# Kernel tuning notes

Measured on AMD Instinct MI355X. Metric: run time of the kernel, lower is better.

The kernel has to match this reference:

```python
import jax, jax.numpy as jnp
import numpy as np


def group_norm(x, g, b, groups, eps=1e-5):
    # x: (B, C, H, W), PyTorch GroupNorm semantics
    B, C, H, W = x.shape
    xr = x.reshape(B, groups, -1)
    m = xr.mean(-1, keepdims=True)
    v = xr.var(-1, keepdims=True)
    xn = ((xr - m) * jax.lax.rsqrt(v + eps)).reshape(B, C, H, W)
    return xn * g[:, None, None] + b[:, None, None]


def mamba(xs, in_w, conv_w, conv_b, xproj_w, dt_w, dt_b, A_log, D, out_w):
    # Standard Mamba block: in_proj -> causal depthwise conv -> SiLU ->
    # x_proj -> softplus(dt_proj) -> selective scan -> gate -> out_proj.
    Bsz, L, d = xs.shape
    di = in_w.shape[0] // 2
    r = dt_w.shape[1]
    n = A_log.shape[1]
    K = conv_w.shape[1]
    xz = xs @ in_w.T                           # (B, L, 2*di)
    xpart, z = xz[..., :di], xz[..., di:]
    xp = jnp.pad(xpart, ((0, 0), (K - 1, 0), (0, 0)))  # causal pad
    xc = conv_b + sum(xp[:, k:k + L, :] * conv_w[:, k] for k in range(K))
    xc = jax.nn.silu(xc)
    proj = xc @ xproj_w.T                      # (B, L, r + 2n)
    dt = proj[..., :r]
    Bm = proj[..., r:r + n]
    Cm = proj[..., r + n:]
    delta = jax.nn.softplus(dt @ dt_w.T + dt_b)   # (B, L, di)
    A = -jnp.exp(A_log)                            # (di, n)
    dA = jnp.exp(jnp.einsum('bld,dn->bldn', delta, A))
    dBu = jnp.einsum('bld,bln,bld->bldn', delta, Bm, xc)

    def step(h, inp):
        dA_t, dBu_t, C_t = inp
        h = dA_t * h + dBu_t                  # (B, di, n)
        return h, jnp.einsum('bdn,bn->bd', h, C_t)

    h0 = jnp.zeros((Bsz, di, n), xs.dtype)
    _, ys = jax.lax.scan(step, h0, (jnp.moveaxis(dA, 1, 0), jnp.moveaxis(dBu, 1, 0), jnp.moveaxis(Cm, 1, 0)))
    y = jnp.moveaxis(ys, 0, 1) + D * xc
    y = y * jax.nn.silu(z)
    return y @ out_w.T


def setup_inputs() -> dict:
    def nrm(i, shape, s=0.05):
        return jax.random.normal(jax.random.fold_in(jax.random.key(0), i), shape, dtype=jnp.float32) * s

    f32 = jnp.float32
    C = 128
    di, r, n = 256, 8, 16          # spa mamba: d_model=128, expand=2
    di2, r2 = 64, 2                # spe mamba: d_model=32
    A1 = jnp.log(jnp.broadcast_to(jnp.arange(1, n + 1, dtype=f32), (di, n)))
    A2 = jnp.log(jnp.broadcast_to(jnp.arange(1, n + 1, dtype=f32), (di2, n)))
    return {
        'x': nrm(0, (2, C, 64, 64), 1.0),
        'pe_w': nrm(1, (C, C)), 'pe_b': jnp.zeros((C,), f32),
        'pe_gn_g': jnp.ones((C,), f32), 'pe_gn_b': jnp.zeros((C,), f32),
        'spa_in_w': nrm(2, (2 * di, C)),
        'spa_conv_w': nrm(3, (di, 4)), 'spa_conv_b': jnp.zeros((di,), f32),
        'spa_xproj_w': nrm(4, (r + 2 * n, di)),
        'spa_dt_w': nrm(5, (di, r)), 'spa_dt_b': jnp.full((di,), -2.0, f32),
        'spa_Alog': A1, 'spa_D': jnp.ones((di,), f32),
        'spa_out_w': nrm(6, (C, di)),
        'spa_gn_g': jnp.ones((C,), f32), 'spa_gn_b': jnp.zeros((C,), f32),
        'spe_in_w': nrm(7, (2 * di2, 32)),
        'spe_conv_w': nrm(8, (di2, 4)), 'spe_conv_b': jnp.zeros((di2,), f32),
        'spe_xproj_w': nrm(9, (r2 + 2 * n, di2)),
        'spe_dt_w': nrm(10, (di2, r2)), 'spe_dt_b': jnp.full((di2,), -2.0, f32),
        'spe_Alog': A2, 'spe_D': jnp.ones((di2,), f32),
        'spe_out_w': nrm(11, (32, di2)),
        'spe_gn_g': jnp.ones((C,), f32), 'spe_gn_b': jnp.zeros((C,), f32),
        'fuse_w': jnp.full((2,), 0.5, f32),
        'cls_w': nrm(12, (10, C)), 'cls_b': jnp.zeros((10,), f32),
        'ref_dw_w': nrm(13, (C, 1, 3, 3)),
        'ref_gn_g': jnp.ones((C,), f32), 'ref_gn_b': jnp.zeros((C,), f32),
        'ref_pw_w': nrm(14, (1, C)), 'ref_pw_b': jnp.zeros((1,), f32),
        'alpha': jnp.asarray(1e-4, f32),
    }


def reference(x, pe_w, pe_b, pe_gn_g, pe_gn_b, spa_in_w, spa_conv_w, spa_conv_b, spa_xproj_w, spa_dt_w, spa_dt_b, spa_Alog, spa_D, spa_out_w, spa_gn_g, spa_gn_b, spe_in_w, spe_conv_w, spe_conv_b, spe_xproj_w, spe_dt_w, spe_dt_b, spe_Alog, spe_D, spe_out_w, spe_gn_g, spe_gn_b, fuse_w, cls_w, cls_b, ref_dw_w, ref_gn_g, ref_gn_b, ref_pw_w, ref_pw_b, alpha):
    B, _, H, W = x.shape
    # patch embedding: 1x1 conv + GroupNorm + SiLU
    h1 = jnp.einsum('bchw,oc->bohw', x, pe_w) + pe_b[:, None, None]
    h1 = jax.nn.silu(group_norm(h1, pe_gn_g, pe_gn_b, 4))
    # SpaMamba: scan over flattened spatial tokens (B, H*W, C)
    seq = h1.transpose(0, 2, 3, 1).reshape(B, H * W, -1)
    y = mamba(seq, spa_in_w, spa_conv_w, spa_conv_b, spa_xproj_w, spa_dt_w, spa_dt_b, spa_Alog, spa_D, spa_out_w)
    y = y.reshape(B, H, W, -1).transpose(0, 3, 1, 2)
    spa = jax.nn.silu(group_norm(y, spa_gn_g, spa_gn_b, 4)) + h1
    # SpeMamba: token_num=4, group_channel_num=32, channel_num=128 (no pad)
    seq2 = h1.transpose(0, 2, 3, 1).reshape(B * H * W, 4, 32)
    y2 = mamba(seq2, spe_in_w, spe_conv_w, spe_conv_b, spe_xproj_w, spe_dt_w, spe_dt_b, spe_Alog, spe_D, spe_out_w)
    y2 = y2.reshape(B, H, W, -1).transpose(0, 3, 1, 2)
    spe = h1 + jax.nn.silu(group_norm(y2, spe_gn_g, spe_gn_b, 4))
    # attention-weighted fusion + residual (BothMamba, use_att=True)
    wts = jax.nn.softmax(fuse_w)
    feat = spa * wts[0] + spe * wts[1] + h1
    # classifier head (1x1 conv)
    logits = jnp.einsum('bchw,oc->bohw', feat, cls_w) + cls_b[:, None, None]
    # BoundaryAwareLogitRefiner
    edge = jax.lax.conv_general_dilated(feat, ref_dw_w, (1, 1), ((1, 1), (1, 1)), feature_group_count=feat.shape[1], dimension_numbers=('NCHW', 'OIHW', 'NCHW'))
    edge = jax.nn.silu(group_norm(edge, ref_gn_g, ref_gn_b, 4))
    edge = jax.nn.sigmoid(jnp.einsum('bchw,oc->bohw', edge, ref_pw_w) + ref_pw_b[:, None, None])
    local = jax.lax.reduce_window(logits, 0.0, jax.lax.add, (1, 1, 3, 3), (1, 1, 1, 1), ((0, 0), (0, 0), (1, 1), (1, 1))) / 9.0  # count_include_pad=True
    return logits + alpha * (1.0 - edge) * (local - logits)
```

## Files before the change

kernel.cpp:

```cpp
#include <hip/hip_runtime.h>
#include <math.h>

#define DEV __device__ __forceinline__

DEV float sigm(float x){ return 1.f/(1.f+__expf(-x)); }
DEV float siluf(float x){ return x * sigm(x); }
DEV float softplusf(float x){ return x > 20.f ? x : log1pf(__expf(x)); }

static constexpr float NG = 131072.0f;
static constexpr float LOG2E = 1.4426950408889634f;

static constexpr size_t WS_H1    = 0;
static constexpr size_t WS_H1PRE = 1048576;
static constexpr size_t WS_XC    = 2097152;
static constexpr size_t WS_ZSIL  = 4194304;
static constexpr size_t WS_XZ    = 6291456;
static constexpr size_t WS_QOFF  = 6619136;
static constexpr size_t WS_LOG   = 8650752;
static constexpr size_t WS_Y     = 10485760;
static constexpr size_t WS_POFF  = 12582912;
static constexpr size_t WS_Y2    = 14155776;
static constexpr size_t WS_FEAT  = 15204352;
static constexpr size_t WS_STATS = 16252928;

__global__ void __launch_bounds__(256)
k_red(const float* __restrict__ part, float* __restrict__ outS, int half){
  __shared__ float red[4];
  int b = blockIdx.x >> 3, j = blockIdx.x & 7;
  float s = 0.f;
  for (int i = b*half + threadIdx.x; i < (b+1)*half; i += 256)
    s += part[(size_t)i*8 + j];
  s += __shfl_xor(s,1); s += __shfl_xor(s,2); s += __shfl_xor(s,4);
  s += __shfl_xor(s,8); s += __shfl_xor(s,16); s += __shfl_xor(s,32);
  if ((threadIdx.x & 63) == 0) red[threadIdx.x>>6] = s;
  __syncthreads();
  if (threadIdx.x == 0) outS[b*8+j] = red[0]+red[1]+red[2]+red[3];
}

__global__ void __launch_bounds__(256)
k_pe(const float* __restrict__ x, const float* __restrict__ pe_w,
     const float* __restrict__ pe_b, float* __restrict__ h1pre,
     float* __restrict__ part){
  __shared__ float As[16][36];
  __shared__ float Bs[16][64];
  __shared__ float red1[2][4], red2[2][4];
  int tid = threadIdx.x;
  int nx = blockIdx.x, my = blockIdx.y;
  int m0 = my*32, n0 = nx*64;
  int b = m0 >> 12, pl0 = m0 & 4095;
  int tx = tid & 15, ty = tid >> 4;
  float acc[2][4];
  #pragma unroll
  for (int i = 0; i < 2; i++)
    #pragma unroll
    for (int j = 0; j < 4; j++) acc[i][j] = 0.f;
  for (int k0 = 0; k0 < 128; k0 += 16){
    if (tid < 128){
      int k = tid >> 3, mm = (tid & 7)*4;
      float4 a = *(const float4*)(x + ((size_t)b*128 + k0+k)*4096 + pl0 + mm);
      *(float4*)&As[k][mm] = a;
    }
    {
      int n = tid >> 2, kq = (tid & 3)*4;
      float4 a = *(const float4*)(pe_w + (size_t)(n0+n)*128 + k0 + kq);
      Bs[kq+0][n] = a.x; Bs[kq+1][n] = a.y; Bs[kq+2][n] = a.z; Bs[kq+3][n] = a.w;
    }
    __syncthreads();
    #pragma unroll
    for (int k = 0; k < 16; k++){
      float2 av = *(const float2*)&As[k][ty*2];
      float4 bv = *(const float4*)&Bs[k][tx*4];
      acc[0][0] += av.x*bv.x; acc[0][1] += av.x*bv.y; acc[0][2] += av.x*bv.z; acc[0][3] += av.x*bv.w;
      acc[1][0] += av.y*bv.x; acc[1][1] += av.y*bv.y; acc[1][2] += av.y*bv.z; acc[1][3] += av.y*bv.w;
    }
    __syncthreads();
  }
  float4 bias = *(const float4*)(pe_b + n0 + tx*4);
  float s1 = 0.f, s2 = 0.f;
  #pragma unroll
  for (int i = 0; i < 2; i++){
    float4 st;
    st.x = acc[i][0]+bias.x; st.y = acc[i][1]+bias.y;
    st.z = acc[i][2]+bias.z; st.w = acc[i][3]+bias.w;
    s1 += st.x+st.y+st.z+st.w;
    s2 += st.x*st.x + st.y*st.y + st.z*st.z + st.w*st.w;
    *(float4*)(h1pre + (size_t)(m0 + ty*2 + i)*128 + n0 + tx*4) = st;
  }
  s1 += __shfl_xor(s1,1);  s2 += __shfl_xor(s2,1);
  s1 += __shfl_xor(s1,2);  s2 += __shfl_xor(s2,2);
  s1 += __shfl_xor(s1,4);  s2 += __shfl_xor(s2,4);
  s1 += __shfl_xor(s1,16); s2 += __shfl_xor(s2,16);
  s1 += __shfl_xor(s1,32); s2 += __shfl_xor(s2,32);
  int lane = tid & 63, w = tid >> 6;
  if ((lane & 55) == 0){
    int gl = (lane >> 3) & 1;
    red1[gl][w] = s1; red2[gl][w] = s2;
  }
  __syncthreads();
  if (tid < 8){
    int gg = tid >> 1, which = tid & 1;
    int gl = gg - nx*2;
    float v = 0.f;
    if (gl == 0 || gl == 1){
      v = which ? (red2[gl][0]+red2[gl][1]+red2[gl][2]+red2[gl][3])
                : (red1[gl][0]+red1[gl][1]+red1[gl][2]+red1[gl][3]);
    }
    int pblk = b*256 + (my & 127)*2 + nx;
    part[(size_t)pblk*8 + tid] = v;
  }
}

__global__ void __launch_bounds__(256)
k_xz(const float* __restrict__ h1pre, const float* __restrict__ in_w,
     const float* __restrict__ stats, const float* __restrict__ gng,
     const float* __restrict__ gnb, float* __restrict__ h1,
     float* __restrict__ xz, float* __restrict__ zsil){
  __shared__ float As[16][68];
  __shared__ float Bs[16][64];
  int tid = threadIdx.x;
  int m0 = blockIdx.y*64, n0 = blockIdx.x*64;
  int tx = tid & 15, ty = tid >> 4;
  float acc[4][4];
  #pragma unroll
  for (int i = 0; i < 4; i++)
    #pragma unroll
    for (int j = 0; j < 4; j++) acc[i][j] = 0.f;
  for (int k0 = 0; k0 < 128; k0 += 16){
    {
      int m = tid >> 2, kk = (tid & 3)*4;
      int pixm = m0 + m, c0 = k0 + kk;
      int bb = pixm >> 12, g = c0 >> 5;
      float4 a = *(const float4*)(h1pre + (size_t)pixm*128 + c0);
      float mu = stats[(bb*4+g)*2] * (1.f/NG);
      float var = stats[(bb*4+g)*2+1] * (1.f/NG) - mu*mu;
      float rs = rsqrtf(var + 1e-5f);
      float4 gg = *(const float4*)(gng + c0);
      float4 gb = *(const float4*)(gnb + c0);
      float4 v;
      v.x = siluf((a.x-mu)*rs*gg.x + gb.x);
      v.y = siluf((a.y-mu)*rs*gg.y + gb.y);
      v.z = siluf((a.z-mu)*rs*gg.z + gb.z);
      v.w = siluf((a.w-mu)*rs*gg.w + gb.w);
      As[kk+0][m] = v.x; As[kk+1][m] = v.y; As[kk+2][m] = v.z; As[kk+3][m] = v.w;
      if (blockIdx.x == 0) *(float4*)(h1 + (size_t)pixm*128 + c0) = v;
    }
    {
      int n = tid >> 2, kq = (tid & 3)*4;
      float4 a = *(const float4*)(in_w + (size_t)(n0+n)*128 + k0 + kq);
      Bs[kq+0][n] = a.x; Bs[kq+1][n] = a.y; Bs[kq+2][n] = a.z; Bs[kq+3][n] = a.w;
    }
    __syncthreads();
    #pragma unroll
    for (int k = 0; k < 16; k++){
      float4 av = *(const float4*)&As[k][ty*4];
      float4 bv = *(const float4*)&Bs[k][tx*4];
      acc[0][0] += av.x*bv.x; acc[0][1] += av.x*bv.y; acc[0][2] += av.x*bv.z; acc[0][3] += av.x*bv.w;
      acc[1][0] += av.y*bv.x; acc[1][1] += av.y*bv.y; acc[1][2] += av.y*bv.z; acc[1][3] += av.y*bv.w;
      acc[2][0] += av.z*bv.x; acc[2][1] += av.z*bv.y; acc[2][2] += av.z*bv.z; acc[2][3] += av.z*bv.w;
      acc[3][0] += av.w*bv.x; acc[3][1] += av.w*bv.y; acc[3][2] += av.w*bv.z; acc[3][3] += av.w*bv.w;
    }
    __syncthreads();
  }
  if (n0 < 256){
    #pragma unroll
    for (int i = 0; i < 4; i++){
      float4 st; st.x = acc[i][0]; st.y = acc[i][1]; st.z = acc[i][2]; st.w = acc[i][3];
      *(float4*)(xz + (size_t)(m0 + ty*4 + i)*512 + n0 + tx*4) = st;
    }
  } else {
    #pragma unroll
    for (int i = 0; i < 4; i++){
      float4 st;
      st.x = siluf(acc[i][0]); st.y = siluf(acc[i][1]);
      st.z = siluf(acc[i][2]); st.w = siluf(acc[i][3]);
      *(float4*)(zsil + (size_t)(m0 + ty*4 + i)*256 + (n0-256) + tx*4) = st;
    }
  }
}

__global__ void __launch_bounds__(256)
k_projc(const float* __restrict__ xz, const float* __restrict__ cw,
        const float* __restrict__ cb, const float* __restrict__ xpw,
        float* __restrict__ xc, float* __restrict__ proj){
  __shared__ float xct[16*260];
  int tid = threadIdx.x;
  int m0 = blockIdx.x * 16;
  {
    int slot = tid >> 6, lane = tid & 63;
    int d4 = lane*4;
    float4 cbv = *(const float4*)(cb + d4);
    float4 cw0 = *(const float4*)(cw + (size_t)(d4+0)*4);
    float4 cw1 = *(const float4*)(cw + (size_t)(d4+1)*4);
    float4 cw2 = *(const float4*)(cw + (size_t)(d4+2)*4);
    float4 cw3 = *(const float4*)(cw + (size_t)(d4+3)*4);
    const float* c0p = (const float*)&cw0;
    const float* c1p = (const float*)&cw1;
    const float* c2p = (const float*)&cw2;
    const float* c3p = (const float*)&cw3;
    for (int i = 0; i < 4; i++){
      int t = slot*4 + i;
      int tok = m0 + t;
      int l = tok & 4095;
      float4 acc = cbv;
      #pragma unroll
      for (int k = 0; k < 4; k++){
        int ls = l - 3 + k;
        if (ls >= 0){
          float4 xv = *(const float4*)(xz + (size_t)(tok-3+k)*512 + d4);
          acc.x += xv.x * c0p[k];
          acc.y += xv.y * c1p[k];
          acc.z += xv.z * c2p[k];
          acc.w += xv.w * c3p[k];
        }
      }
      float4 s;
      s.x = siluf(acc.x); s.y = siluf(acc.y); s.z = siluf(acc.z); s.w = siluf(acc.w);
      *(float4*)&xct[t*260 + d4] = s;
      *(float4*)(xc + (size_t)tok*256 + d4) = s;
    }
  }
  __syncthreads();
  {
    int t = tid & 15, jq = tid >> 4;
    int tok = m0 + t;
    float a0 = 0.f, a1 = 0.f, a2 = 0.f;
    for (int k0 = 0; k0 < 256; k0 += 4){
      float4 av = *(const float4*)&xct[t*260 + k0];
      float4 w0 = *(const float4*)(xpw + (size_t)jq*256 + k0);
      float4 w1 = *(const float4*)(xpw + (size_t)(jq+16)*256 + k0);
      a0 += av.x*w0.x + av.y*w0.y + av.z*w0.z + av.w*w0.w;
      a1 += av.x*w1.x + av.y*w1.y + av.z*w1.z + av.w*w1.w;
      if (jq < 8){
        float4 w2 = *(const float4*)(xpw + (size_t)(jq+32)*256 + k0);
        a2 += av.x*w2.x + av.y*w2.y + av.z*w2.z + av.w*w2.w;
      }
    }
    float* pr = proj + (size_t)tok*40;
    pr[jq] = a0;
    pr[jq+16] = a1;
    if (jq < 8) pr[jq+32] = a2;
  }
}

__global__ void __launch_bounds__(256)
k_delta(const float* __restrict__ proj, const float* __restrict__ dtw,
        const float* __restrict__ dtb, float* __restrict__ delta){
  int tid = threadIdx.x;
  int tok = blockIdx.x*4 + (tid >> 6);
  int lane = tid & 63;
  int d0 = lane*4;
  const float4* pr4 = (const float4*)(proj + (size_t)tok*40);
  float4 p0 = pr4[0], p1 = pr4[1];
  float4 outv;
  float* po = (float*)&outv;
  #pragma unroll
  for (int j = 0; j < 4; j++){
    int d = d0 + j;
    const float4* wr = (const float4*)(dtw + (size_t)d*8);
    float4 w0 = wr[0], w1 = wr[1];
    float v = dtb[d] + p0.x*w0.x + p0.y*w0.y + p0.z*w0.z + p0.w*w0.w
                     + p1.x*w1.x + p1.y*w1.y + p1.z*w1.z + p1.w*w1.w;
    po[j] = softplusf(v);
  }
  *(float4*)(delta + (size_t)tok*256 + d0) = outv;
}

__global__ void __launch_bounds__(256)
k_scan1(const float* __restrict__ delta, const float* __restrict__ proj,
        const float* __restrict__ xc, const float* __restrict__ Alog,
        float* __restrict__ P, float* __restrict__ Q){
  int blk = blockIdx.x;
  int dblk = blk & 3;
  int bc = blk >> 2;
  int b = bc >> 8, chunk = bc & 255;
  int tid = threadIdx.x;
  int dl = tid >> 2, ng = tid & 3;
  int d = dblk*64 + dl;
  float4 a4 = *(const float4*)(Alog + (size_t)d*16 + ng*4);
  float An[4] = {-__expf(a4.x)*LOG2E, -__expf(a4.y)*LOG2E,
                 -__expf(a4.z)*LOG2E, -__expf(a4.w)*LOG2E};
  float Pv[4] = {1.f,1.f,1.f,1.f}, Qv[4] = {0.f,0.f,0.f,0.f};
  size_t row0 = (size_t)(b*4096 + chunk*16);
  for (int l = 0; l < 16; l++){
    size_t r = row0 + l;
    float dv = delta[r*256 + d];
    float xv = xc[r*256 + d];
    float4 bm = *(const float4*)(proj + r*40 + 8 + ng*4);
    float dBx = dv*xv;
    float bmv[4] = {bm.x, bm.y, bm.z, bm.w};
    #pragma unroll
    for (int k = 0; k < 4; k++){
      float a = exp2f(dv*An[k]);
      Qv[k] = a*Qv[k] + bmv[k]*dBx;
      Pv[k] *= a;
    }
  }
  size_t o = (size_t)bc*4096 + dblk*1024 + tid*4;
  float4 pv; pv.x=Pv[0]; pv.y=Pv[1]; pv.z=Pv[2]; pv.w=Pv[3];
  float4 qv; qv.x=Qv[0]; qv.y=Qv[1]; qv.z=Qv[2]; qv.w=Qv[3];
  *(float4*)(P + o) = pv;
  *(float4*)(Q + o) = qv;
}

__global__ void __launch_bounds__(256)
k_scan2(const float* __restrict__ P, const float* __restrict__ Q,
        float* __restrict__ hs){
  __shared__ float Ps[256][17], Qs[256][17];
  int tid = threadIdx.x;
  int b = blockIdx.x >> 8;
  int dn0 = (blockIdx.x & 255) * 16;
  for (int i = tid; i < 1024; i += 256){
    int ch = i >> 2, g = (i & 3)*4;
    size_t gaddr = (size_t)(b*256+ch)*4096 + dn0 + g;
    float4 p = *(const float4*)(P + gaddr);
    float4 q = *(const float4*)(Q + gaddr);
    Ps[ch][g]=p.x; Ps[ch][g+1]=p.y; Ps[ch][g+2]=p.z; Ps[ch][g+3]=p.w;
    Qs[ch][g]=q.x; Qs[ch][g+1]=q.y; Qs[ch][g+2]=q.z; Qs[ch][g+3]=q.w;
  }
  __syncthreads();
  int lane = tid & 63, wv = tid >> 6;
  for (int rep = 0; rep < 4; rep++){
    int c = wv*4 + rep;
    float p0 = Ps[4*lane+0][c], q0 = Qs[4*lane+0][c];
    float p1 = Ps[4*lane+1][c], q1 = Qs[4*lane+1][c];
    float p2 = Ps[4*lane+2][c], q2 = Qs[4*lane+2][c];
    float p3 = Ps[4*lane+3][c], q3 = Qs[4*lane+3][c];
    float p = p0, q = q0;
    q = p1*q + q1; p *= p1;
    q = p2*q + q2; p *= p2;
    q = p3*q + q3; p *= p3;
    #pragma unroll
    for (int off = 1; off < 64; off <<= 1){
      float pp = __shfl_up(p, off);
      float qp = __shfl_up(q, off);
      if (lane >= off){ q = p*qp + q; p = p*pp; }
    }
    float h0 = __shfl_up(q, 1);
    if (lane == 0) h0 = 0.f;
    float h1 = p0*h0 + q0;
    float h2 = p1*h1 + q1;
    float h3 = p2*h2 + q2;
    Ps[4*lane+0][c] = h0;
    Ps[4*lane+1][c] = h1;
    Ps[4*lane+2][c] = h2;
    Ps[4*lane+3][c] = h3;
  }
  __syncthreads();
  for (int i = tid; i < 1024; i += 256){
    int ch = i >> 2, g = (i & 3)*4;
    size_t gaddr = (size_t)(b*256+ch)*4096 + dn0 + g;
    float4 h;
    h.x = Ps[ch][g]; h.y = Ps[ch][g+1]; h.z = Ps[ch][g+2]; h.w = Ps[ch][g+3];
    *(float4*)(hs + gaddr) = h;
  }
}

__global__ void __launch_bounds__(256)
k_scan3(const float* __restrict__ delta, const float* __restrict__ proj,
        const float* __restrict__ xc, const float* __restrict__ zsil,
        const float* __restrict__ Alog, const float* __restrict__ Dv,
        const float* __restrict__ hs, float* __restrict__ y){
  int blk = blockIdx.x;
  int dblk = blk & 3;
  int bc = blk >> 2;
  int b = bc >> 8, chunk = bc & 255;
  int tid = threadIdx.x;
  int dl = tid >> 2, ng = tid & 3;
  int d = dblk*64 + dl;
  float4 a4 = *(const float4*)(Alog + (size_t)d*16 + ng*4);
  float An[4] = {-__expf(a4.x)*LOG2E, -__expf(a4.y)*LOG2E,
                 -__expf(a4.z)*LOG2E, -__expf(a4.w)*LOG2E};
  float Dd = Dv[d];
  float h[4];
  {
    size_t o = (size_t)bc*4096 + dblk*1024 + tid*4;
    float4 hv = *(const float4*)(hs + o);
    h[0]=hv.x; h[1]=hv.y; h[2]=hv.z; h[3]=hv.w;
  }
  size_t row0 = (size_t)(b*4096 + chunk*16);
  for (int l = 0; l < 16; l++){
    size_t r = row0 + l;
    float dv = delta[r*256 + d];
    float xv = xc[r*256 + d];
    float4 bm = *(const float4*)(proj + r*40 + 8 + ng*4);
    float4 cm = *(const float4*)(proj + r*40 + 24 + ng*4);
    float dBx = dv*xv;
    float bmv[4] = {bm.x, bm.y, bm.z, bm.w};
    float cmv[4] = {cm.x, cm.y, cm.z, cm.w};
    float ys = 0.f;
    #pragma unroll
    for (int k = 0; k < 4; k++){
      float a = exp2f(dv*An[k]);
      h[k] = a*h[k] + bmv[k]*dBx;
      ys += h[k]*cmv[k];
    }
    ys += __shfl_xor(ys, 1);
    ys += __shfl_xor(ys, 2);
    if (ng == 0){
      float zv = zsil[r*256 + d];
      y[r*256 + d] = (ys + Dd*xv) * zv;
    }
  }
}

__global__ void __launch_bounds__(256)
k_outproj(const float* __restrict__ y, const float* __restrict__ out_w,
          float* __restrict__ yproj, float* __restrict__ part){
  __shared__ float As[16][36];
  __shared__ float Bs[16][64];
  __shared__ float red1[2][4], red2[2][4];
  int tid = threadIdx.x;
  int nx = blockIdx.x, my = blockIdx.y;
  int m0 = my*32, n0 = nx*64;
  int b = m0 >> 12;
  int tx = tid & 15, ty = tid >> 4;
  float acc[2][4];
  #pragma unroll
  for (int i = 0; i < 2; i++)
    #pragma unroll
    for (int j = 0; j < 4; j++) acc[i][j] = 0.f;
  for (int k0 = 0; k0 < 256; k0 += 16){
    if (tid < 128){
      int m = tid >> 2, kk = (tid & 3)*4;
      float4 a = *(const float4*)(y + (size_t)(m0+m)*256 + k0+kk);
      As[kk+0][m] = a.x; As[kk+1][m] = a.y; As[kk+2][m] = a.z; As[kk+3][m] = a.w;
    }
    {
      int n = tid >> 2, kq = (tid & 3)*4;
      float4 a = *(const float4*)(out_w + (size_t)(n0+n)*256 + k0 + kq);
      Bs[kq+0][n] = a.x; Bs[kq+1][n] = a.y; Bs[kq+2][n] = a.z; Bs[kq+3][n] = a.w;
    }
    __syncthreads();
    #pragma unroll
    for (int k = 0; k < 16; k++){
      float2 av = *(const float2*)&As[k][ty*2];
      float4 bv = *(const float4*)&Bs[k][tx*4];
      acc[0][0] += av.x*bv.x; acc[0][1] += av.x*bv.y; acc[0][2] += av.x*bv.z; acc[0][3] += av.x*bv.w;
      acc[1][0] += av.y*bv.x; acc[1][1] += av.y*bv.y; acc[1][2] += av.y*bv.z; acc[1][3] += av.y*bv.w;
    }
    __syncthreads();
  }
  float s1 = 0.f, s2 = 0.f;
  #pragma unroll
  for (int i = 0; i < 2; i++){
    float4 st; st.x = acc[i][0]; st.y = acc[i][1]; st.z = acc[i][2]; st.w = acc[i][3];
    s1 += st.x+st.y+st.z+st.w;
    s2 += st.x*st.x + st.y*st.y + st.z*st.z + st.w*st.w;
    *(float4*)(yproj + (size_t)(m0 + ty*2 + i)*128 + n0 + tx*4) = st;
  }
  s1 += __shfl_xor(s1,1);  s2 += __shfl_xor(s2,1);
  s1 += __shfl_xor(s1,2);  s2 += __shfl_xor(s2,2);
  s1 += __shfl_xor(s1,4);  s2 += __shfl_xor(s2,4);
  s1 += __shfl_xor(s1,16); s2 += __shfl_xor(s2,16);
  s1 += __shfl_xor(s1,32); s2 += __shfl_xor(s2,32);
  int lane = tid & 63, w = tid >> 6;
  if ((lane & 55) == 0){
    int gl = (lane >> 3) & 1;
    red1[gl][w] = s1; red2[gl][w] = s2;
  }
  __syncthreads();
  if (tid < 8){
    int gg = tid >> 1, which = tid & 1;
    int gl = gg - nx*2;
    float v = 0.f;
    if (gl == 0 || gl == 1){
      v = which ? (red2[gl][0]+red2[gl][1]+red2[gl][2]+red2[gl][3])
                : (red1[gl][0]+red1[gl][1]+red1[gl][2]+red1[gl][3]);
    }
    int pblk = b*256 + (my & 127)*2 + nx;
    part[(size_t)pblk*8 + tid] = v;
  }
}

__global__ void __launch_bounds__(256)
k_spe_a(const float* __restrict__ h1, const float* __restrict__ in_w,
        const float* __restrict__ conv_w, const float* __restrict__ conv_b,
        float* __restrict__ xc2, float* __restrict__ xc2T,
        float* __restrict__ zsil2){
  __shared__ float s_in[4][128];
  int tid = threadIdx.x;
  int w = tid >> 6, lane = tid & 63;
  float wx[32], wz[32];
  {
    const float4* rx = (const float4*)(in_w + (size_t)lane*32);
    const float4* rz = (const float4*)(in_w + (size_t)(64+lane)*32);
    #pragma unroll
    for (int k = 0; k < 8; k++){
      float4 a = rx[k]; wx[k*4]=a.x; wx[k*4+1]=a.y; wx[k*4+2]=a.z; wx[k*4+3]=a.w;
      float4 b = rz[k]; wz[k*4]=b.x; wz[k*4+1]=b.y; wz[k*4+2]=b.z; wz[k*4+3]=b.w;
    }
  }
  float4 cwv = ((const float4*)conv_w)[lane];
  float cbv = conv_b[lane];
  for (int i = 0; i < 4; i++){
    int pix = blockIdx.x*16 + w*4 + i;
    float2 hv = ((const float2*)(h1 + (size_t)pix*128))[lane];
    s_in[w][2*lane] = hv.x; s_in[w][2*lane+1] = hv.y;
    float xpr[4], zs[4];
    #pragma unroll
    for (int l = 0; l < 4; l++){
      const float4* sv = (const float4*)&s_in[w][l*32];
      float ax = 0.f, az = 0.f;
      #pragma unroll
      for (int c4 = 0; c4 < 8; c4++){
        float4 v = sv[c4];
        ax += v.x*wx[c4*4] + v.y*wx[c4*4+1] + v.z*wx[c4*4+2] + v.w*wx[c4*4+3];
        az += v.x*wz[c4*4] + v.y*wz[c4*4+1] + v.z*wz[c4*4+2] + v.w*wz[c4*4+3];
      }
      xpr[l] = ax; zs[l] = siluf(az);
    }
    #pragma unroll
    for (int l = 0; l < 4; l++){
      float v = cbv;
      if (l >= 3) v += xpr[l-3]*cwv.x;
      if (l >= 2) v += xpr[l-2]*cwv.y;
      if (l >= 1) v += xpr[l-1]*cwv.z;
      v += xpr[l]*cwv.w;
      float sx = siluf(v);
      int tok = pix*4 + l;
      xc2 [(size_t)tok*64 + lane] = sx;
      xc2T[(size_t)lane*32768 + tok] = sx;
      zsil2[(size_t)tok*64 + lane] = zs[l];
    }
  }
}

__global__ void __launch_bounds__(256)
k_spe_b(const float* __restrict__ xc2T, const float* __restrict__ xpw,
        float* __restrict__ proj){
  int tok = blockIdx.x*256 + threadIdx.x;
  float xcv[64];
  #pragma unroll 64
  for (int dd = 0; dd < 64; dd++) xcv[dd] = xc2T[(size_t)dd*32768 + tok];
  float* pr = proj + (size_t)tok*36;
  #pragma unroll 2
  for (int j = 0; j < 34; j++){
    const float4* wr = (const float4*)(xpw + j*64);
    float a = 0.f;
    #pragma unroll
    for (int k = 0; k < 16; k++){
      float4 wv = wr[k];
      a += xcv[k*4]*wv.x + xcv[k*4+1]*wv.y + xcv[k*4+2]*wv.z + xcv[k*4+3]*wv.w;
    }
    pr[j] = a;
  }
}

__global__ void __launch_bounds__(256)
k_spe_c(const float* __restrict__ xc2, const float* __restrict__ zsil2,
        const float* __restrict__ proj, const float* __restrict__ dt_w,
        const float* __restrict__ dt_b, const float* __restrict__ Alog,
        const float* __restrict__ Dvec, float* __restrict__ yg){
  int tid = threadIdx.x;
  int w = tid >> 6, lane = tid & 63;
  float2 dtwv = ((const float2*)dt_w)[lane];
  float dbv = dt_b[lane], Dd = Dvec[lane];
  float An[16];
  {
    const float4* ar = (const float4*)(Alog + (size_t)lane*16);
    #pragma unroll
    for (int k = 0; k < 4; k++){
      float4 a = ar[k];
      An[k*4]   = -__expf(a.x)*LOG2E; An[k*4+1] = -__expf(a.y)*LOG2E;
      An[k*4+2] = -__expf(a.z)*LOG2E; An[k*4+3] = -__expf(a.w)*LOG2E;
    }
  }
  for (int i = 0; i < 4; i++){
    int pix = blockIdx.x*16 + w*4 + i;
    float h[16];
    #pragma unroll
    for (int n = 0; n < 16; n++) h[n] = 0.f;
    #pragma unroll
    for (int l = 0; l < 4; l++){
      int tok = pix*4 + l;
      float pj[36];
      {
        const float4* pr = (const float4*)(proj + (size_t)tok*36);
        #pragma unroll
        for (int k = 0; k < 9; k++){
          float4 v = pr[k];
          pj[k*4]=v.x; pj[k*4+1]=v.y; pj[k*4+2]=v.z; pj[k*4+3]=v.w;
        }
      }
      float xv = xc2[(size_t)tok*64 + lane];
      float zv = zsil2[(size_t)tok*64 + lane];
      float dt = softplusf(dbv + pj[0]*dtwv.x + pj[1]*dtwv.y);
      float ys = 0.f;
      #pragma unroll
      for (int n = 0; n < 16; n++){
        float a = exp2f(dt * An[n]);
        h[n] = a*h[n] + dt * pj[2+n] * xv;
        ys += h[n] * pj[18+n];
      }
      yg[(size_t)tok*64 + lane] = (ys + Dd*xv) * zv;
    }
  }
}

__global__ void __launch_bounds__(256)
k_spe_d(const float* __restrict__ yg, const float* __restrict__ out_w,
        float* __restrict__ y2, float* __restrict__ part){
  __shared__ float ldsWT[64*32];
  __shared__ float bst[8];
  int tid = threadIdx.x;
  for (int i = tid; i < 2048; i += 256){
    int c2 = i >> 6, dd = i & 63;
    ldsWT[dd*32 + c2] = out_w[i];
  }
  if (tid < 8) bst[tid] = 0.f;
  __syncthreads();
  int w = tid >> 6, lane = tid & 63;
  int c2 = lane & 31, slot = lane >> 5;
  int tokbase = blockIdx.x*64 + w*16 + slot;
  float acc[8];
  #pragma unroll
  for (int i = 0; i < 8; i++) acc[i] = 0.f;
  for (int dd4 = 0; dd4 < 16; dd4++){
    float w0 = ldsWT[(dd4*4+0)*32 + c2];
    float w1 = ldsWT[(dd4*4+1)*32 + c2];
    float w2 = ldsWT[(dd4*4+2)*32 + c2];
    float w3 = ldsWT[(dd4*4+3)*32 + c2];
    #pragma unroll
    for (int i = 0; i < 8; i++){
      int tok = tokbase + 2*i;
      float4 yv = ((const float4*)(yg + (size_t)tok*64))[dd4];
      acc[i] += yv.x*w0 + yv.y*w1 + yv.z*w2 + yv.w*w3;
    }
  }
  #pragma unroll
  for (int i = 0; i < 8; i++){
    int tok = tokbase + 2*i;
    int pix = tok >> 2, l = tok & 3;
    y2[(size_t)pix*128 + l*32 + c2] = acc[i];
    float s1 = acc[i], s2 = acc[i]*acc[i];
    s1 += __shfl_xor(s1,1);  s2 += __shfl_xor(s2,1);
    s1 += __shfl_xor(s1,2);  s2 += __shfl_xor(s2,2);
    s1 += __shfl_xor(s1,4);  s2 += __shfl_xor(s2,4);
    s1 += __shfl_xor(s1,8);  s2 += __shfl_xor(s2,8);
    s1 += __shfl_xor(s1,16); s2 += __shfl_xor(s2,16);
    if (c2 == 0){
      atomicAdd(&bst[l*2+0], s1);
      atomicAdd(&bst[l*2+1], s2);
    }
  }
  __syncthreads();
  if (tid < 8) part[(size_t)blockIdx.x*8 + tid] = bst[tid];
}

__global__ void __launch_bounds__(256)
k_fuse(const float* __restrict__ h1, const float* __restrict__ yproj,
       const float* __restrict__ y2, const float* __restrict__ stats,
       const float* __restrict__ spa_g, const float* __restrict__ spa_b,
       const float* __restrict__ spe_g, const float* __restrict__ spe_b,
       const float* __restrict__ fuse_w, const float* __restrict__ cls_w,
       const float* __restrict__ cls_b, float* __restrict__ feat,
       float* __restrict__ logits){
  __shared__ float ft[2][128];
  int tid = threadIdx.x;
  int pixl = tid >> 7, c = tid & 127;
  int pix = blockIdx.x*2 + pixl;
  int b = pix >> 12, g = c >> 5;
  float m1 = stats[16 + (b*4+g)*2]   * (1.f/NG);
  float v1 = stats[16 + (b*4+g)*2+1] * (1.f/NG) - m1*m1;
  float m2 = stats[32 + (b*4+g)*2]   * (1.f/NG);
  float v2 = stats[32 + (b*4+g)*2+1] * (1.f/NG) - m2*m2;
  float h = h1[(size_t)pix*128 + c];
  float sa = siluf((yproj[(size_t)pix*128+c] - m1)*rsqrtf(v1+1e-5f)*spa_g[c] + spa_b[c]) + h;
  float sp = h + siluf((y2[(size_t)pix*128+c] - m2)*rsqrtf(v2+1e-5f)*spe_g[c] + spe_b[c]);
  float e0 = __expf(fuse_w[0]), e1 = __expf(fuse_w[1]);
  float w0 = e0/(e0+e1), w1 = e1/(e0+e1);
  float f = sa*w0 + sp*w1 + h;
  feat[(size_t)pix*128+c] = f;
  ft[pixl][c] = f;
  __syncthreads();
  if (tid < 20){
    int pl = (tid >= 10) ? 1 : 0;
    int o = tid - pl*10;
    float acc = cls_b[o];
    for (int cc = 0; cc < 128; cc++) acc += ft[pl][cc]*cls_w[o*128+cc];
    logits[(size_t)(blockIdx.x*2 + pl)*16 + o] = acc;
  }
}

__global__ void __launch_bounds__(256)
k_dw(const float* __restrict__ feat, const float* __restrict__ dww,
     float* __restrict__ epre, float* __restrict__ part){
  __shared__ float ft[100*128];
  __shared__ float red1[4][64], red2[4][64];
  int tid = threadIdx.x;
  int blk = blockIdx.x;
  int b = blk >> 6, ty = (blk >> 3) & 7, tx = blk & 7;
  for (int idx = tid; idx < 100*128; idx += 256){
    int row = idx >> 7, c = idx & 127;
    int r10 = row / 10, c10 = row - r10*10;
    int ry = ty*8 + r10 - 1, rx = tx*8 + c10 - 1;
    float v = 0.f;
    if (ry >= 0 && ry < 64 && rx >= 0 && rx < 64)
      v = feat[(size_t)((b<<12)|(ry<<6)|rx)*128 + c];
    ft[idx] = v;
  }
  __syncthreads();
  int c = tid & 127, pl = tid >> 7;
  float w[9];
  #pragma unroll
  for (int k = 0; k < 9; k++) w[k] = dww[c*9+k];
  float s1 = 0.f, s2 = 0.f;
  for (int i = 0; i < 32; i++){
    int pixl = i*2 + pl;
    int py = pixl >> 3, px = pixl & 7;
    float acc = 0.f;
    #pragma unroll
    for (int dy = 0; dy < 3; dy++)
      #pragma unroll
      for (int dx = 0; dx < 3; dx++)
        acc += ft[((py+dy)*10 + (px+dx))*128 + c] * w[dy*3+dx];
    epre[(size_t)((b<<12)|((ty*8+py)<<6)|(tx*8+px))*128 + c] = acc;
    s1 += acc; s2 += acc*acc;
  }
  int g = c >> 5;
  int idx = (c & 31) | (pl << 5);
  red1[g][idx] = s1; red2[g][idx] = s2;
  __syncthreads();
  int rg = tid >> 6, ridx = tid & 63;
  for (int s = 32; s >= 1; s >>= 1){
    if (ridx < s){ red1[rg][ridx] += red1[rg][ridx+s]; red2[rg][ridx] += red2[rg][ridx+s]; }
    __syncthreads();
  }
  if (ridx == 0){
    part[(size_t)blk*8 + rg*2+0] = red1[rg][0];
    part[(size_t)blk*8 + rg*2+1] = red2[rg][0];
  }
}

__global__ void __launch_bounds__(256)
k_final(const float* __restrict__ epre, const float* __restrict__ logits,
        const float* __restrict__ stats, const float* __restrict__ rg_g,
        const float* __restrict__ rg_b, const float* __restrict__ pw_w,
        const float* __restrict__ pw_b, const float* __restrict__ alpha,
        float* __restrict__ outp){
  __shared__ float part[4];
  __shared__ float edge_s[2];
  int tid = threadIdx.x;
  int pixl = tid >> 7, c = tid & 127;
  int pix = blockIdx.x*2 + pixl;
  int b = pix >> 12, p = pix & 4095, yy = p >> 6, xx = p & 63;
  int g = c >> 5;
  float m = stats[48 + (b*4+g)*2]   * (1.f/NG);
  float v = stats[48 + (b*4+g)*2+1] * (1.f/NG) - m*m;
  float e = epre[(size_t)pix*128+c];
  float en = siluf((e-m)*rsqrtf(v+1e-5f)*rg_g[c] + rg_b[c]);
  float pv = en * pw_w[c];
  pv += __shfl_xor(pv,1);  pv += __shfl_xor(pv,2);  pv += __shfl_xor(pv,4);
  pv += __shfl_xor(pv,8);  pv += __shfl_xor(pv,16); pv += __shfl_xor(pv,32);
  if ((tid & 63) == 0) part[tid>>6] = pv;
  __syncthreads();
  if (tid < 2) edge_s[tid] = sigm(part[tid*2] + part[tid*2+1] + pw_b[0]);
  __syncthreads();
  if (c < 10){
    float ed = edge_s[pixl];
    int o = c;
    float lg = logits[(size_t)pix*16 + o];
    float loc = 0.f;
    for (int dy = -1; dy <= 1; dy++){
      int ny = yy+dy; if (ny < 0 || ny > 63) continue;
      for (int dx = -1; dx <= 1; dx++){
        int nx = xx+dx; if (nx < 0 || nx > 63) continue;
        loc += logits[(size_t)((b<<12)|(ny<<6)|nx)*16 + o];
      }
    }
    loc *= (1.f/9.f);
    outp[(size_t)((b*10+o)<<12) + p] = lg + alpha[0]*(1.f-ed)*(loc - lg);
  }
}

extern "C" void kernel_launch(void* const* d_in, const int* in_sizes, int n_in,
                              void* d_out, int out_size, void* d_ws, size_t ws_size,
                              hipStream_t stream){
  const float* x          = (const float*)d_in[0];
  const float* pe_w       = (const float*)d_in[1];
  const float* pe_b       = (const float*)d_in[2];
  const float* pe_gn_g    = (const float*)d_in[3];
  const float* pe_gn_b    = (const float*)d_in[4];
  const float* spa_in_w   = (const float*)d_in[5];
  const float* spa_conv_w = (const float*)d_in[6];
  const float* spa_conv_b = (const float*)d_in[7];
  const float* spa_xproj_w= (const float*)d_in[8];
  const float* spa_dt_w   = (const float*)d_in[9];
  const float* spa_dt_b   = (const float*)d_in[10];
  const float* spa_Alog   = (const float*)d_in[11];
  const float* spa_D      = (const float*)d_in[12];
  const float* spa_out_w  = (const float*)d_in[13];
  const float* spa_gn_g   = (const float*)d_in[14];
  const float* spa_gn_b   = (const float*)d_in[15];
  const float* spe_in_w   = (const float*)d_in[16];
  const float* spe_conv_w = (const float*)d_in[17];
  const float* spe_conv_b = (const float*)d_in[18];
  const float* spe_xproj_w= (const float*)d_in[19];
  const float* spe_dt_w   = (const float*)d_in[20];
  const float* spe_dt_b   = (const float*)d_in[21];
  const float* spe_Alog   = (const float*)d_in[22];
  const float* spe_D      = (const float*)d_in[23];
  const float* spe_out_w  = (const float*)d_in[24];
  const float* spe_gn_g   = (const float*)d_in[25];
  const float* spe_gn_b   = (const float*)d_in[26];
  const float* fuse_w     = (const float*)d_in[27];
  const float* cls_w      = (const float*)d_in[28];
  const float* cls_b      = (const float*)d_in[29];
  const float* ref_dw_w   = (const float*)d_in[30];
  const float* ref_gn_g   = (const float*)d_in[31];
  const float* ref_gn_b   = (const float*)d_in[32];
  const float* ref_pw_w   = (const float*)d_in[33];
  const float* ref_pw_b   = (const float*)d_in[34];
  const float* alpha      = (const float*)d_in[35];
  float* ws  = (float*)d_ws;
  float* out = (float*)d_out;

  float* Pb    = ws + WS_POFF;
  float* Qb    = ws + WS_QOFF;
  float* HSb   = Pb;
  float* dely  = ws + WS_Y;
  float* partPE  = ws + WS_Y;
  float* partSPA = ws + WS_POFF;
  float* partSPE = ws + WS_POFF + 16384;
  float* partDW  = ws + WS_POFF + 65536;
  float* proj  = ws + WS_FEAT;
  float* xc2   = ws + WS_XC;
  float* xc2T  = ws + WS_ZSIL;
  float* zsil2 = ws + WS_XZ;
  float* proj2 = ws + WS_XZ + 2097152;
  float* yg    = ws + WS_Y;

  k_pe<<<dim3(2,256),256,0,stream>>>(x, pe_w, pe_b, ws+WS_H1PRE, partPE);
  k_red<<<16,256,0,stream>>>(partPE, ws+WS_STATS+0, 256);
  k_xz<<<dim3(8,128),256,0,stream>>>(ws+WS_H1PRE, spa_in_w, ws+WS_STATS,
      pe_gn_g, pe_gn_b, ws+WS_H1, ws+WS_XZ, ws+WS_ZSIL);
  k_projc<<<512,256,0,stream>>>(ws+WS_XZ, spa_conv_w, spa_conv_b, spa_xproj_w,
      ws+WS_XC, proj);
  k_delta<<<2048,256,0,stream>>>(proj, spa_dt_w, spa_dt_b, dely);
  k_scan1<<<2048,256,0,stream>>>(dely, proj, ws+WS_XC, spa_Alog, Pb, Qb);
  k_scan2<<<512,256,0,stream>>>(Pb, Qb, HSb);
  k_scan3<<<2048,256,0,stream>>>(dely, proj, ws+WS_XC, ws+WS_ZSIL,
      spa_Alog, spa_D, HSb, dely);
  k_outproj<<<dim3(2,256),256,0,stream>>>(dely, spa_out_w, ws+WS_H1PRE, partSPA);
  k_red<<<16,256,0,stream>>>(partSPA, ws+WS_STATS+16, 256);
  k_spe_a<<<512,256,0,stream>>>(ws+WS_H1, spe_in_w, spe_conv_w, spe_conv_b,
      xc2, xc2T, zsil2);
  k_spe_b<<<128,256,0,stream>>>(xc2T, spe_xproj_w, proj2);
  k_spe_c<<<512,256,0,stream>>>(xc2, zsil2, proj2, spe_dt_w, spe_dt_b,
      spe_Alog, spe_D, yg);
  k_spe_d<<<512,256,0,stream>>>(yg, spe_out_w, ws+WS_Y2, partSPE);
  k_red<<<16,256,0,stream>>>(partSPE, ws+WS_STATS+32, 256);
  k_fuse<<<4096,256,0,stream>>>(ws+WS_H1, ws+WS_H1PRE, ws+WS_Y2, ws+WS_STATS,
      spa_gn_g, spa_gn_b, spe_gn_g, spe_gn_b, fuse_w, cls_w, cls_b,
      ws+WS_FEAT, ws+WS_LOG);
  k_dw<<<128,256,0,stream>>>(ws+WS_FEAT, ref_dw_w, ws+WS_Y, partDW);
  k_red<<<16,256,0,stream>>>(partDW, ws+WS_STATS+48, 64);
  k_final<<<4096,256,0,stream>>>(ws+WS_Y, ws+WS_LOG, ws+WS_STATS,
      ref_gn_g, ref_gn_b, ref_pw_w, ref_pw_b, alpha, out);
  (void)in_sizes; (void)n_in; (void)out_size; (void)ws_size;
}
```

Baseline: 384.1 us.

## Fuse small reductions and projection kernels to cut launch count

Removes four standalone group-norm stat reduction launches. Each consumer block (k_xz, k_final) now reduces the partial sums redundantly into shared memory, and the remaining two reductions are merged into one k_red2 launch. k_delta is folded into k_projc, so dt_proj+softplus runs from shared memory. k_spe_a and k_spe_b are merged into k_spe_ab, which computes x_proj from a shared tile and drops the transposed xc2T buffer. The aim is fewer launches and less intermediate traffic. The cost is redundant reduction work in every block of k_xz (1024 blocks) and k_final (4096 blocks), plus a less coalesced delta write and x_proj weight loads from global memory.

```diff
diff --git a/kernel.cpp b/kernel.cpp
--- a/kernel.cpp
+++ b/kernel.cpp
@@ -23,18 +23,17 @@
 static constexpr size_t WS_FEAT  = 15204352;
 static constexpr size_t WS_STATS = 16252928;
 
-__global__ void __launch_bounds__(256)
-k_red(const float* __restrict__ part, float* __restrict__ outS, int half){
-  __shared__ float red[4];
-  int b = blockIdx.x >> 3, j = blockIdx.x & 7;
+DEV void reduce_part(const float* __restrict__ part, int rowsPerB, float* sst){
+  int tid = threadIdx.x;
+  int p = tid >> 4, sl = tid & 15;
+  int b = p >> 3, j = p & 7;
   float s = 0.f;
-  for (int i = b*half + threadIdx.x; i < (b+1)*half; i += 256)
-    s += part[(size_t)i*8 + j];
-  s += __shfl_xor(s,1); s += __shfl_xor(s,2); s += __shfl_xor(s,4);
-  s += __shfl_xor(s,8); s += __shfl_xor(s,16); s += __shfl_xor(s,32);
-  if ((threadIdx.x & 63) == 0) red[threadIdx.x>>6] = s;
-  __syncthreads();
-  if (threadIdx.x == 0) outS[b*8+j] = red[0]+red[1]+red[2]+red[3];
+  for (int row = sl; row < rowsPerB; row += 16)
+    s += part[((size_t)b*rowsPerB + row)*8 + j];
+  s += __shfl_xor(s,1); s += __shfl_xor(s,2);
+  s += __shfl_xor(s,4); s += __shfl_xor(s,8);
+  if (sl == 0) sst[p] = s;
+  __syncthreads();
 }
 
 __global__ void __launch_bounds__(256)
@@ -112,11 +111,13 @@
 
 __global__ void __launch_bounds__(256)
 k_xz(const float* __restrict__ h1pre, const float* __restrict__ in_w,
-     const float* __restrict__ stats, const float* __restrict__ gng,
+     const float* __restrict__ partPE, const float* __restrict__ gng,
      const float* __restrict__ gnb, float* __restrict__ h1,
      float* __restrict__ xz, float* __restrict__ zsil){
   __shared__ float As[16][68];
   __shared__ float Bs[16][64];
+  __shared__ float sst[16];
+  reduce_part(partPE, 256, sst);
   int tid = threadIdx.x;
   int m0 = blockIdx.y*64, n0 = blockIdx.x*64;
   int tx = tid & 15, ty = tid >> 4;
@@ -131,8 +132,8 @@
       int pixm = m0 + m, c0 = k0 + kk;
       int bb = pixm >> 12, g = c0 >> 5;
       float4 a = *(const float4*)(h1pre + (size_t)pixm*128 + c0);
-      float mu = stats[(bb*4+g)*2] * (1.f/NG);
-      float var = stats[(bb*4+g)*2+1] * (1.f/NG) - mu*mu;
+      float mu = sst[bb*8 + g*2] * (1.f/NG);
+      float var = sst[bb*8 + g*2 + 1] * (1.f/NG) - mu*mu;
       float rs = rsqrtf(var + 1e-5f);
       float4 gg = *(const float4*)(gng + c0);
       float4 gb = *(const float4*)(gnb + c0);
@@ -181,8 +182,11 @@
 __global__ void __launch_bounds__(256)
 k_projc(const float* __restrict__ xz, const float* __restrict__ cw,
         const float* __restrict__ cb, const float* __restrict__ xpw,
-        float* __restrict__ xc, float* __restrict__ proj){
+        const float* __restrict__ dtw, const float* __restrict__ dtb,
+        float* __restrict__ xc, float* __restrict__ proj,
+        float* __restrict__ delta){
   __shared__ float xct[16*260];
+  __shared__ float s_dt[16][9];
   int tid = threadIdx.x;
   int m0 = blockIdx.x * 16;
   {
@@ -238,31 +242,20 @@
     float* pr = proj + (size_t)tok*40;
     pr[jq] = a0;
     pr[jq+16] = a1;
-    if (jq < 8) pr[jq+32] = a2;
-  }
-}
-
-__global__ void __launch_bounds__(256)
-k_delta(const float* __restrict__ proj, const float* __restrict__ dtw,
-        const float* __restrict__ dtb, float* __restrict__ delta){
-  int tid = threadIdx.x;
-  int tok = blockIdx.x*4 + (tid >> 6);
-  int lane = tid & 63;
-  int d0 = lane*4;
-  const float4* pr4 = (const float4*)(proj + (size_t)tok*40);
-  float4 p0 = pr4[0], p1 = pr4[1];
-  float4 outv;
-  float* po = (float*)&outv;
-  #pragma unroll
-  for (int j = 0; j < 4; j++){
-    int d = d0 + j;
+    if (jq < 8){ pr[jq+32] = a2; s_dt[t][jq] = a0; }
+  }
+  __syncthreads();
+  {
+    int d = tid;
     const float4* wr = (const float4*)(dtw + (size_t)d*8);
     float4 w0 = wr[0], w1 = wr[1];
-    float v = dtb[d] + p0.x*w0.x + p0.y*w0.y + p0.z*w0.z + p0.w*w0.w
-                     + p1.x*w1.x + p1.y*w1.y + p1.z*w1.z + p1.w*w1.w;
-    po[j] = softplusf(v);
-  }
-  *(float4*)(delta + (size_t)tok*256 + d0) = outv;
+    float bd = dtb[d];
+    for (int t = 0; t < 16; t++){
+      float v = bd + s_dt[t][0]*w0.x + s_dt[t][1]*w0.y + s_dt[t][2]*w0.z + s_dt[t][3]*w0.w
+                   + s_dt[t][4]*w1.x + s_dt[t][5]*w1.y + s_dt[t][6]*w1.z + s_dt[t][7]*w1.w;
+      delta[(size_t)(m0+t)*256 + d] = softplusf(v);
+    }
+  }
 }
 
 __global__ void __launch_bounds__(256)
@@ -473,15 +466,16 @@
 }
 
 __global__ void __launch_bounds__(256)
-k_spe_a(const float* __restrict__ h1, const float* __restrict__ in_w,
-        const float* __restrict__ conv_w, const float* __restrict__ conv_b,
-        float* __restrict__ xc2, float* __restrict__ xc2T,
-        float* __restrict__ zsil2){
+k_spe_ab(const float* __restrict__ h1, const float* __restrict__ in_w,
+         const float* __restrict__ conv_w, const float* __restrict__ conv_b,
+         const float* __restrict__ xpw, float* __restrict__ xc2,
+         float* __restrict__ zsil2, float* __restrict__ proj2){
   __shared__ float s_in[4][128];
+  __shared__ float s_xc[64][66];
   int tid = threadIdx.x;
   int w = tid >> 6, lane = tid & 63;
-  float wx[32], wz[32];
   {
+    float wx[32], wz[32];
     const float4* rx = (const float4*)(in_w + (size_t)lane*32);
     const float4* rz = (const float4*)(in_w + (size_t)(64+lane)*32);
     #pragma unroll
@@ -489,60 +483,61 @@
       float4 a = rx[k]; wx[k*4]=a.x; wx[k*4+1]=a.y; wx[k*4+2]=a.z; wx[k*4+3]=a.w;
       float4 b = rz[k]; wz[k*4]=b.x; wz[k*4+1]=b.y; wz[k*4+2]=b.z; wz[k*4+3]=b.w;
     }
-  }
-  float4 cwv = ((const float4*)conv_w)[lane];
-  float cbv = conv_b[lane];
-  for (int i = 0; i < 4; i++){
-    int pix = blockIdx.x*16 + w*4 + i;
-    float2 hv = ((const float2*)(h1 + (size_t)pix*128))[lane];
-    s_in[w][2*lane] = hv.x; s_in[w][2*lane+1] = hv.y;
-    float xpr[4], zs[4];
-    #pragma unroll
-    for (int l = 0; l < 4; l++){
-      const float4* sv = (const float4*)&s_in[w][l*32];
-      float ax = 0.f, az = 0.f;
+    float4 cwv = ((const float4*)conv_w)[lane];
+    float cbv = conv_b[lane];
+    for (int i = 0; i < 4; i++){
+      int pix = blockIdx.x*16 + w*4 + i;
+      float2 hv = ((const float2*)(h1 + (size_t)pix*128))[lane];
+      s_in[w][2*lane] = hv.x; s_in[w][2*lane+1] = hv.y;
+      float xpr[4], zs[4];
       #pragma unroll
-      for (int c4 = 0; c4 < 8; c4++){
-        float4 v = sv[c4];
-        ax += v.x*wx[c4*4] + v.y*wx[c4*4+1] + v.z*wx[c4*4+2] + v.w*wx[c4*4+3];
-        az += v.x*wz[c4*4] + v.y*wz[c4*4+1] + v.z*wz[c4*4+2] + v.w*wz[c4*4+3];
+      for (int l = 0; l < 4; l++){
+        const float4* sv = (const float4*)&s_in[w][l*32];
+        float ax = 0.f, az = 0.f;
+        #pragma unroll
+        for (int c4 = 0; c4 < 8; c4++){
+          float4 v = sv[c4];
+          ax += v.x*wx[c4*4] + v.y*wx[c4*4+1] + v.z*wx[c4*4+2] + v.w*wx[c4*4+3];
+          az += v.x*wz[c4*4] + v.y*wz[c4*4+1] + v.z*wz[c4*4+2] + v.w*wz[c4*4+3];
+        }
+        xpr[l] = ax; zs[l] = siluf(az);
       }
-      xpr[l] = ax; zs[l] = siluf(az);
-    }
-    #pragma unroll
-    for (int l = 0; l < 4; l++){
-      float v = cbv;
-      if (l >= 3) v += xpr[l-3]*cwv.x;
-      if (l >= 2) v += xpr[l-2]*cwv.y;
-      if (l >= 1) v += xpr[l-1]*cwv.z;
-      v += xpr[l]*cwv.w;
-      float sx = siluf(v);
-      int tok = pix*4 + l;
-      xc2 [(size_t)tok*64 + lane] = sx;
-      xc2T[(size_t)lane*32768 + tok] = sx;
-      zsil2[(size_t)tok*64 + lane] = zs[l];
-    }
-  }
-}
-
-__global__ void __launch_bounds__(256)
-k_spe_b(const float* __restrict__ xc2T, const float* __restrict__ xpw,
-        float* __restrict__ proj){
-  int tok = blockIdx.x*256 + threadIdx.x;
-  float xcv[64];
-  #pragma unroll 64
-  for (int dd = 0; dd < 64; dd++) xcv[dd] = xc2T[(size_t)dd*32768 + tok];
-  float* pr = proj + (size_t)tok*36;
-  #pragma unroll 2
-  for (int j = 0; j < 34; j++){
-    const float4* wr = (const float4*)(xpw + j*64);
-    float a = 0.f;
-    #pragma unroll
-    for (int k = 0; k < 16; k++){
-      float4 wv = wr[k];
-      a += xcv[k*4]*wv.x + xcv[k*4+1]*wv.y + xcv[k*4+2]*wv.z + xcv[k*4+3]*wv.w;
-    }
-    pr[j] = a;
+      #pragma unroll
+      for (int l = 0; l < 4; l++){
+        float v = cbv;
+        if (l >= 3) v += xpr[l-3]*cwv.x;
+        if (l >= 2) v += xpr[l-2]*cwv.y;
+        if (l >= 1) v += xpr[l-1]*cwv.z;
+        v += xpr[l]*cwv.w;
+        float sx = siluf(v);
+        int t = (w*4+i)*4 + l;
+        int tok = blockIdx.x*64 + t;
+        s_xc[t][lane] = sx;
+        xc2 [(size_t)tok*64 + lane] = sx;
+        zsil2[(size_t)tok*64 + lane] = zs[l];
+      }
+    }
+  }
+  __syncthreads();
+  {
+    int t = lane;
+    float a[9];
+    #pragma unroll
+    for (int j = 0; j < 9; j++) a[j] = 0.f;
+    for (int k = 0; k < 64; k++){
+      float xk = s_xc[t][k];
+      #pragma unroll
+      for (int j = 0; j < 9; j++){
+        int ja = w*9 + j; if (ja > 33) ja = 33;
+        a[j] += xk * xpw[(size_t)ja*64 + k];
+      }
+    }
+    float* pr = proj2 + (size_t)(blockIdx.x*64 + t)*36;
+    #pragma unroll
+    for (int j = 0; j < 9; j++){
+      int ja = w*9 + j;
+      if (ja < 34) pr[ja] = a[j];
+    }
   }
 }
 
@@ -648,6 +643,25 @@
 }
 
 __global__ void __launch_bounds__(256)
+k_red2(const float* __restrict__ pa, const float* __restrict__ pb,
+       float* __restrict__ outS){
+  __shared__ float red[4];
+  int bid = blockIdx.x;
+  const float* part = (bid < 16) ? pa : pb;
+  float* dst = outS + ((bid < 16) ? 0 : 16);
+  int id = bid & 15;
+  int b = id >> 3, j = id & 7;
+  float s = 0.f;
+  for (int i = b*256 + threadIdx.x; i < (b+1)*256; i += 256)
+    s += part[(size_t)i*8 + j];
+  s += __shfl_xor(s,1); s += __shfl_xor(s,2); s += __shfl_xor(s,4);
+  s += __shfl_xor(s,8); s += __shfl_xor(s,16); s += __shfl_xor(s,32);
+  if ((threadIdx.x & 63) == 0) red[threadIdx.x>>6] = s;
+  __syncthreads();
+  if (threadIdx.x == 0) dst[b*8+j] = red[0]+red[1]+red[2]+red[3];
+}
+
+__global__ void __launch_bounds__(256)
 k_fuse(const float* __restrict__ h1, const float* __restrict__ yproj,
        const float* __restrict__ y2, const float* __restrict__ stats,
        const float* __restrict__ spa_g, const float* __restrict__ spa_b,
@@ -734,19 +748,21 @@
 
 __global__ void __launch_bounds__(256)
 k_final(const float* __restrict__ epre, const float* __restrict__ logits,
-        const float* __restrict__ stats, const float* __restrict__ rg_g,
+        const float* __restrict__ partDW, const float* __restrict__ rg_g,
         const float* __restrict__ rg_b, const float* __restrict__ pw_w,
         const float* __restrict__ pw_b, const float* __restrict__ alpha,
         float* __restrict__ outp){
+  __shared__ float sst[16];
   __shared__ float part[4];
   __shared__ float edge_s[2];
+  reduce_part(partDW, 64, sst);
   int tid = threadIdx.x;
   int pixl = tid >> 7, c = tid & 127;
   int pix = blockIdx.x*2 + pixl;
   int b = pix >> 12, p = pix & 4095, yy = p >> 6, xx = p & 63;
   int g = c >> 5;
-  float m = stats[48 + (b*4+g)*2]   * (1.f/NG);
-  float v = stats[48 + (b*4+g)*2+1] * (1.f/NG) - m*m;
+  float m = sst[b*8 + g*2]   * (1.f/NG);
+  float v = sst[b*8 + g*2+1] * (1.f/NG) - m*m;
   float e = epre[(size_t)pix*128+c];
   float en = siluf((e-m)*rsqrtf(v+1e-5f)*rg_g[c] + rg_b[c]);
   float pv = en * pw_w[c];
@@ -825,37 +841,31 @@
   float* partDW  = ws + WS_POFF + 65536;
   float* proj  = ws + WS_FEAT;
   float* xc2   = ws + WS_XC;
-  float* xc2T  = ws + WS_ZSIL;
   float* zsil2 = ws + WS_XZ;
   float* proj2 = ws + WS_XZ + 2097152;
   float* yg    = ws + WS_Y;
 
   k_pe<<<dim3(2,256),256,0,stream>>>(x, pe_w, pe_b, ws+WS_H1PRE, partPE);
-  k_red<<<16,256,0,stream>>>(partPE, ws+WS_STATS+0, 256);
-  k_xz<<<dim3(8,128),256,0,stream>>>(ws+WS_H1PRE, spa_in_w, ws+WS_STATS,
+  k_xz<<<dim3(8,128),256,0,stream>>>(ws+WS_H1PRE, spa_in_w, partPE,
       pe_gn_g, pe_gn_b, ws+WS_H1, ws+WS_XZ, ws+WS_ZSIL);
   k_projc<<<512,256,0,stream>>>(ws+WS_XZ, spa_conv_w, spa_conv_b, spa_xproj_w,
-      ws+WS_XC, proj);
-  k_delta<<<2048,256,0,stream>>>(proj, spa_dt_w, spa_dt_b, dely);
+      spa_dt_w, spa_dt_b, ws+WS_XC, proj, dely);
   k_scan1<<<2048,256,0,stream>>>(dely, proj, ws+WS_XC, spa_Alog, Pb, Qb);
   k_scan2<<<512,256,0,stream>>>(Pb, Qb, HSb);
   k_scan3<<<2048,256,0,stream>>>(dely, proj, ws+WS_XC, ws+WS_ZSIL,
       spa_Alog, spa_D, HSb, dely);
   k_outproj<<<dim3(2,256),256,0,stream>>>(dely, spa_out_w, ws+WS_H1PRE, partSPA);
-  k_red<<<16,256,0,stream>>>(partSPA, ws+WS_STATS+16, 256);
-  k_spe_a<<<512,256,0,stream>>>(ws+WS_H1, spe_in_w, spe_conv_w, spe_conv_b,
-      xc2, xc2T, zsil2);
-  k_spe_b<<<128,256,0,stream>>>(xc2T, spe_xproj_w, proj2);
+  k_spe_ab<<<512,256,0,stream>>>(ws+WS_H1, spe_in_w, spe_conv_w, spe_conv_b,
+      spe_xproj_w, xc2, zsil2, proj2);
   k_spe_c<<<512,256,0,stream>>>(xc2, zsil2, proj2, spe_dt_w, spe_dt_b,
       spe_Alog, spe_D, yg);
   k_spe_d<<<512,256,0,stream>>>(yg, spe_out_w, ws+WS_Y2, partSPE);
-  k_red<<<16,256,0,stream>>>(partSPE, ws+WS_STATS+32, 256);
+  k_red2<<<32,256,0,stream>>>(partSPA, partSPE, ws+WS_STATS+16);
   k_fuse<<<4096,256,0,stream>>>(ws+WS_H1, ws+WS_H1PRE, ws+WS_Y2, ws+WS_STATS,
       spa_gn_g, spa_gn_b, spe_gn_g, spe_gn_b, fuse_w, cls_w, cls_b,
       ws+WS_FEAT, ws+WS_LOG);
   k_dw<<<128,256,0,stream>>>(ws+WS_FEAT, ref_dw_w, ws+WS_Y, partDW);
-  k_red<<<16,256,0,stream>>>(partDW, ws+WS_STATS+48, 64);
-  k_final<<<4096,256,0,stream>>>(ws+WS_Y, ws+WS_LOG, ws+WS_STATS,
+  k_final<<<4096,256,0,stream>>>(ws+WS_Y, ws+WS_LOG, partDW,
       ref_gn_g, ref_gn_b, ref_pw_w, ref_pw_b, alpha, out);
   (void)in_sizes; (void)n_in; (void)out_size; (void)ws_size;
 }
```

Result: faster. 373.6 us (-2.7%).
